# Kernel optimization log

Measured on AMD Instinct MI355X. Metric: run time of the kernel, lower is better.

## Reference

```python
import jax, jax.numpy as jnp
import numpy as np

R = 12          # resolution (H = W = G); L = R**3 = 1728
HEADS = 12


def setup_inputs() -> dict:
    key = jax.random.key(0)
    k1, k2, k3 = jax.random.split(key, 3)
    B, L, C = 4, R ** 3, 768
    qkv = jax.random.normal(k1, (3, B, L, C), dtype=jnp.float32)
    lepe_w = jax.random.normal(k2, (C, 1, 3, 3, 3), dtype=jnp.float32) * 0.05
    lepe_b = jax.random.normal(k3, (C,), dtype=jnp.float32) * 0.01
    return {"qkv": qkv, "lepe_w": lepe_w, "lepe_b": lepe_b}


def reference(qkv, lepe_w, lepe_b):
    # qkv: [3, B, L, C]; idx=0 => window == full volume, so attention is dense over L.
    q, k, v = qkv[0], qkv[1], qkv[2]
    B, L, C = q.shape
    hd = C // HEADS
    scale = hd ** -0.5

    # im2cswin with full-volume window preserves token order: [B, L, C] -> [B, H, L, d]
    qh = q.reshape(B, L, HEADS, hd).transpose(0, 2, 1, 3)
    kh = k.reshape(B, L, HEADS, hd).transpose(0, 2, 1, 3)

    # get_lepe: v -> [B, C, R, R, R], depthwise 3x3x3 conv (groups=C)
    v_img = v.transpose(0, 2, 1).reshape(B, C, R, R, R)
    lepe = jax.lax.conv_general_dilated(
        v_img, lepe_w, window_strides=(1, 1, 1), padding="SAME",
        dimension_numbers=("NCDHW", "OIDHW", "NCDHW"), feature_group_count=C,
    ) + lepe_b[None, :, None, None, None]
    lepe = lepe.reshape(B, HEADS, hd, L).transpose(0, 1, 3, 2)   # [B, H, L, d]
    vh = v_img.reshape(B, HEADS, hd, L).transpose(0, 1, 3, 2)    # [B, H, L, d]

    attn = jax.nn.softmax(jnp.einsum("bhqd,bhkd->bhqk", qh * scale, kh), axis=-1)
    out = jnp.einsum("bhqk,bhkd->bhqd", attn, vh) + lepe          # [B, H, L, d]

    # windows2img with full window is an inverse reshape back to [B, L, C]
    return out.transpose(0, 2, 1, 3).reshape(B, L, C)
```

## Files before the change

kernel.cpp:

```cpp
#include <hip/hip_runtime.h>

#define RR 12
#define LL 1728
#define CC 768
#define HEADS 12
#define HD 64
#define BATCH 4

typedef __attribute__((ext_vector_type(8))) short bf8;
typedef __attribute__((ext_vector_type(4))) float f4;

__device__ inline unsigned short f2bf(float x) {
  unsigned int u = __float_as_uint(x);
  return (unsigned short)((u + 0x7FFFu + ((u >> 16) & 1u)) >> 16);
}
__device__ inline unsigned short f2bfr(float x) {
  return (unsigned short)((__float_as_uint(x) + 0x8000u) >> 16);
}

__device__ inline float fast_exp2(float x) {
#if __has_builtin(__builtin_amdgcn_exp2f)
  return __builtin_amdgcn_exp2f(x);
#else
  return exp2f(x);
#endif
}

__device__ inline void gld16(const unsigned short* g, unsigned short* l) {
  __builtin_amdgcn_global_load_lds((const __attribute__((address_space(1))) unsigned int*)g,
                                   (__attribute__((address_space(3))) unsigned int*)l, 16, 0, 0);
}

#define QSCALE 0.1803368801111244f

__global__ __launch_bounds__(256) void prep_kernel(const float* __restrict__ qkv,
                                                   unsigned short* __restrict__ qb,
                                                   unsigned short* __restrict__ kb,
                                                   unsigned short* __restrict__ vT) {
  __shared__ unsigned short tl[64 * 65];
  const int lt = blockIdx.x;
  const int h = blockIdx.y;
  const int b = blockIdx.z;
  const int t = threadIdx.x;

  {
    const int r0 = t >> 4;
    const int c4 = (t & 15) * 4;
#pragma unroll
    for (int p = 0; p < 4; ++p) {
      const int row = lt * 64 + p * 16 + r0;
      const size_t off = ((size_t)b * LL + row) * CC + h * HD + c4;
      const float4 qv = *(const float4*)(qkv + off);
      ushort4 oq;
      oq.x = f2bf(qv.x * QSCALE); oq.y = f2bf(qv.y * QSCALE);
      oq.z = f2bf(qv.z * QSCALE); oq.w = f2bf(qv.w * QSCALE);
      *(ushort4*)(qb + off) = oq;
      const float4 kv = *(const float4*)(qkv + (size_t)BATCH * LL * CC + off);
      ushort4 ok;
      ok.x = f2bf(kv.x); ok.y = f2bf(kv.y); ok.z = f2bf(kv.z); ok.w = f2bf(kv.w);
      *(ushort4*)(kb + off) = ok;
    }
  }

  const float* vsrc = qkv + ((size_t)(2 * BATCH + b)) * LL * CC;
#pragma unroll
  for (int it = 0; it < 4; ++it) {
    const int idx = it * 256 + t;
    const int lrow = idx >> 4;
    const int c4 = (idx & 15) * 4;
    const float4 vv = *(const float4*)(vsrc + (size_t)(lt * 64 + lrow) * CC + h * HD + c4);
    tl[(c4 + 0) * 65 + lrow] = f2bf(vv.x);
    tl[(c4 + 1) * 65 + lrow] = f2bf(vv.y);
    tl[(c4 + 2) * 65 + lrow] = f2bf(vv.z);
    tl[(c4 + 3) * 65 + lrow] = f2bf(vv.w);
  }
  __syncthreads();
#pragma unroll
  for (int it = 0; it < 4; ++it) {
    const int idx = it * 256 + t;
    const int drow = idx >> 4;
    const int s4 = (idx & 15) * 4;
    const int lb = s4 >> 2;
    ushort4 o;
    o.x = tl[drow * 65 + lb];
    o.y = tl[drow * 65 + 16 + lb];
    o.z = tl[drow * 65 + 32 + lb];
    o.w = tl[drow * 65 + 48 + lb];
    *(ushort4*)(vT + (((size_t)(b * HEADS + h) * HD + drow) * LL) + lt * 64 + s4) = o;
  }
}

__global__ __launch_bounds__(256) void lepe_kernel(const float* __restrict__ qkv,
                                                   const float* __restrict__ w,
                                                   const float* __restrict__ bias,
                                                   float* __restrict__ out) {
  __shared__ float w_lds[256 * 27];

  const int z = blockIdx.x / RR;
  const int y = blockIdx.x % RR;
  const int c0 = blockIdx.y * 256;
  const int c = c0 + threadIdx.x;
  const int b = blockIdx.z;
  const float* vb = qkv + ((size_t)(2 * BATCH + b)) * LL * CC + c;

  {
    const float* wsrc = w + (size_t)c0 * 27;
#pragma unroll
    for (int i = 0; i < 7; ++i) {
      const int idx = i * 256 + threadIdx.x;
      if (idx < 1728)
        *(float4*)&w_lds[idx * 4] = *(const float4*)&wsrc[idx * 4];
    }
  }
  __syncthreads();

  float wreg[27];
#pragma unroll
  for (int j = 0; j < 27; ++j) wreg[j] = w_lds[threadIdx.x * 27 + j];
  const float bv = bias[c];

  int loff[9];
  bool lval[9];
#pragma unroll
  for (int dz = 0; dz < 3; ++dz)
#pragma unroll
    for (int dy = 0; dy < 3; ++dy) {
      const int i = dz * 3 + dy;
      const int zz = z + dz - 1, yy = y + dy - 1;
      lval[i] = (zz >= 0 && zz < RR && yy >= 0 && yy < RR);
      loff[i] = lval[i] ? ((zz * RR + yy) * RR) * CC : 0;
    }

  float prev[9], cur[9], nxt[9];
#pragma unroll
  for (int i = 0; i < 9; ++i) {
    prev[i] = 0.f;
    cur[i] = lval[i] ? vb[loff[i]] : 0.f;
    nxt[i] = lval[i] ? vb[loff[i] + CC] : 0.f;
  }

  const size_t obase = ((size_t)b * LL + (z * RR + y) * RR) * CC + c;
#pragma unroll
  for (int x = 0; x < RR; ++x) {
    float acc = bv;
#pragma unroll
    for (int i = 0; i < 9; ++i)
      acc += wreg[i * 3] * prev[i] + wreg[i * 3 + 1] * cur[i] + wreg[i * 3 + 2] * nxt[i];
    out[obase + (size_t)x * CC] = acc;
#pragma unroll
    for (int i = 0; i < 9; ++i) {
      prev[i] = cur[i];
      cur[i] = nxt[i];
      nxt[i] = (x + 2 < RR && lval[i]) ? vb[loff[i] + (x + 2) * CC] : 0.f;
    }
  }
}

__global__ __launch_bounds__(256) void attn_kernel(const unsigned short* __restrict__ qb,
                                                   const unsigned short* __restrict__ kb,
                                                   const unsigned short* __restrict__ vT,
                                                   float* __restrict__ out) {
  __shared__ unsigned short k_lds[2][64 * 64];
  __shared__ unsigned short v_lds[2][64 * 64];
  __shared__ unsigned short p_lds[4][16 * 72];

  const int qt = blockIdx.x;
  const int h = blockIdx.y;
  const int b = blockIdx.z;
  const int t = threadIdx.x;
  const int lane = t & 63;
  const int wave = t >> 6;
  const int m = lane & 15;
  const int quad = lane >> 4;

  bf8 qf[2];
  {
    const size_t qbase = ((size_t)(b * LL + qt * 64 + wave * 16 + m)) * CC + h * HD;
    qf[0] = *(const bf8*)(qb + qbase + quad * 8);
    qf[1] = *(const bf8*)(qb + qbase + 32 + quad * 8);
  }

  int koff[2], voff[2], ldsb[2];
#pragma unroll
  for (int j = 0; j < 2; ++j) {
    const int cidx = (j * 4 + wave) * 64 + lane;
    const int row = cidx >> 3;
    const int sc = (cidx & 7) ^ (row & 7);
    koff[j] = row * CC + sc * 8;
    voff[j] = row * LL + sc * 8;
    ldsb[j] = (j * 4 + wave) * 512;
  }

  const unsigned short* kgb = kb + (size_t)b * LL * CC + h * HD;
  const unsigned short* vgb = vT + ((size_t)(b * HEADS + h) * HD) * LL;

  gld16(kgb + koff[0], &k_lds[0][ldsb[0]]);
  gld16(kgb + koff[1], &k_lds[0][ldsb[1]]);
  gld16(vgb + voff[0], &v_lds[0][ldsb[0]]);
  gld16(vgb + voff[1], &v_lds[0][ldsb[1]]);

  f4 o_acc[4] = {};
  float psum[4] = {0.f, 0.f, 0.f, 0.f};

#define ATTN_BODY(KT, CUR)                                                              \
  {                                                                                     \
    __syncthreads();            \
    if ((KT) < 26) {                                                                    \
      const size_t ko = (size_t)((KT) + 1) * 64 * CC;                                   \
      const int vo = ((KT) + 1) * 64;                                                   \
      gld16(kgb + ko + koff[0], &k_lds[(CUR) ^ 1][ldsb[0]]);                            \
      gld16(kgb + ko + koff[1], &k_lds[(CUR) ^ 1][ldsb[1]]);                            \
      gld16(vgb + vo + voff[0], &v_lds[(CUR) ^ 1][ldsb[0]]);                            \
      gld16(vgb + vo + voff[1], &v_lds[(CUR) ^ 1][ldsb[1]]);                            \
    }                                                                                   \
    f4 s_acc[4] = {};                                                                   \
    _Pragma("unroll")                                                                   \
    for (int nt = 0; nt < 4; ++nt) {                                                    \
      _Pragma("unroll")                                                                 \
      for (int ks = 0; ks < 2; ++ks) {                                                  \
        const int cc = ((ks * 4 + quad) ^ (m & 7)) * 8;                                 \
        const bf8 kf = *(const bf8*)&k_lds[CUR][(nt * 16 + m) * 64 + cc];               \
        s_acc[nt] = __builtin_amdgcn_mfma_f32_16x16x32_bf16(qf[ks], kf, s_acc[nt], 0, 0, 0); \
      }                                                                                 \
    }                                                                                   \
    _Pragma("unroll")                                                                   \
    for (int r = 0; r < 4; ++r) {                                                       \
      const float p0 = fast_exp2(s_acc[0][r]);                                          \
      const float p1 = fast_exp2(s_acc[1][r]);                                          \
      const float p2 = fast_exp2(s_acc[2][r]);                                          \
      const float p3 = fast_exp2(s_acc[3][r]);                                          \
      psum[r] += (p0 + p1) + (p2 + p3);                                                 \
      ushort4 pk;        \
      pk.x = f2bfr(p0); pk.y = f2bfr(p1); pk.z = f2bfr(p2); pk.w = f2bfr(p3);           \
      *(ushort4*)&p_lds[wave][(quad * 4 + r) * 72 + m * 4] = pk;                        \
    }                                                                                   \
    __asm__ volatile("s_waitcnt lgkmcnt(0)" ::: "memory");      \
    bf8 pf[2];                                                                          \
    _Pragma("unroll")                                                                   \
    for (int ks = 0; ks < 2; ++ks)                                                      \
      pf[ks] = *(const bf8*)&p_lds[wave][m * 72 + ks * 32 + quad * 8];                  \
    _Pragma("unroll")                                                                   \
    for (int nt = 0; nt < 4; ++nt) {                                                    \
      _Pragma("unroll")                                                                 \
      for (int ks = 0; ks < 2; ++ks) {                                                  \
        const int cc = ((ks * 4 + quad) ^ (m & 7)) * 8;                                 \
        const bf8 vf = *(const bf8*)&v_lds[CUR][(nt * 16 + m) * 64 + cc];               \
        o_acc[nt] = __builtin_amdgcn_mfma_f32_16x16x32_bf16(pf[ks], vf, o_acc[nt], 0, 0, 0); \
      }                                                                                 \
    }                                                                                   \
  }

  for (int ktp = 0; ktp < 13; ++ktp) {
    const int kt0 = ktp * 2;
    ATTN_BODY(kt0, 0)
    ATTN_BODY(kt0 + 1, 1)
  }
  ATTN_BODY(26, 0)
#undef ATTN_BODY

#pragma unroll
  for (int r = 0; r < 4; ++r) {
    float s = psum[r];
    s += __shfl_xor(s, 1);
    s += __shfl_xor(s, 2);
    s += __shfl_xor(s, 4);
    s += __shfl_xor(s, 8);
    const float inv = 1.0f / s;
    const int row = qt * 64 + wave * 16 + quad * 4 + r;
    float* op = out + ((size_t)b * LL + row) * CC + h * HD;
#pragma unroll
    for (int nt = 0; nt < 4; ++nt) {
      const int cix = nt * 16 + m;
      op[cix] = op[cix] + o_acc[nt][r] * inv;
    }
  }
}

extern "C" void kernel_launch(void* const* d_in, const int* in_sizes, int n_in,
                              void* d_out, int out_size, void* d_ws, size_t ws_size,
                              hipStream_t stream) {
  (void)in_sizes; (void)n_in; (void)ws_size; (void)out_size;
  const float* qkv = (const float*)d_in[0];
  const float* lepe_w = (const float*)d_in[1];
  const float* lepe_b = (const float*)d_in[2];
  float* out = (float*)d_out;

  const size_t NE = (size_t)BATCH * LL * CC;
  unsigned short* qb = (unsigned short*)d_ws;
  unsigned short* kb = qb + NE;
  unsigned short* vT = kb + NE;

  prep_kernel<<<dim3(27, HEADS, BATCH), 256, 0, stream>>>(qkv, qb, kb, vT);
  lepe_kernel<<<dim3(RR * RR, CC / 256, BATCH), 256, 0, stream>>>(qkv, lepe_w, lepe_b, out);
  attn_kernel<<<dim3(27, HEADS, BATCH), 256, 0, stream>>>(qb, kb, vT, out);
}
```

Measured before the change: 195.6 us.

## Fuse depthwise LePE convolution into the attention kernel's key-tile loop

New measurement: 275.5 us. 1.41x slower.

```diff
diff --git a/kernel.cpp b/kernel.cpp
--- a/kernel.cpp
+++ b/kernel.cpp
@@ -90,79 +90,17 @@
   }
 }
 
-__global__ __launch_bounds__(256) void lepe_kernel(const float* __restrict__ qkv,
-                                                   const float* __restrict__ w,
-                                                   const float* __restrict__ bias,
-                                                   float* __restrict__ out) {
-  __shared__ float w_lds[256 * 27];
-
-  const int z = blockIdx.x / RR;
-  const int y = blockIdx.x % RR;
-  const int c0 = blockIdx.y * 256;
-  const int c = c0 + threadIdx.x;
-  const int b = blockIdx.z;
-  const float* vb = qkv + ((size_t)(2 * BATCH + b)) * LL * CC + c;
-
-  {
-    const float* wsrc = w + (size_t)c0 * 27;
-#pragma unroll
-    for (int i = 0; i < 7; ++i) {
-      const int idx = i * 256 + threadIdx.x;
-      if (idx < 1728)
-        *(float4*)&w_lds[idx * 4] = *(const float4*)&wsrc[idx * 4];
-    }
-  }
-  __syncthreads();
-
-  float wreg[27];
-#pragma unroll
-  for (int j = 0; j < 27; ++j) wreg[j] = w_lds[threadIdx.x * 27 + j];
-  const float bv = bias[c];
-
-  int loff[9];
-  bool lval[9];
-#pragma unroll
-  for (int dz = 0; dz < 3; ++dz)
-#pragma unroll
-    for (int dy = 0; dy < 3; ++dy) {
-      const int i = dz * 3 + dy;
-      const int zz = z + dz - 1, yy = y + dy - 1;
-      lval[i] = (zz >= 0 && zz < RR && yy >= 0 && yy < RR);
-      loff[i] = lval[i] ? ((zz * RR + yy) * RR) * CC : 0;
-    }
-
-  float prev[9], cur[9], nxt[9];
-#pragma unroll
-  for (int i = 0; i < 9; ++i) {
-    prev[i] = 0.f;
-    cur[i] = lval[i] ? vb[loff[i]] : 0.f;
-    nxt[i] = lval[i] ? vb[loff[i] + CC] : 0.f;
-  }
-
-  const size_t obase = ((size_t)b * LL + (z * RR + y) * RR) * CC + c;
-#pragma unroll
-  for (int x = 0; x < RR; ++x) {
-    float acc = bv;
-#pragma unroll
-    for (int i = 0; i < 9; ++i)
-      acc += wreg[i * 3] * prev[i] + wreg[i * 3 + 1] * cur[i] + wreg[i * 3 + 2] * nxt[i];
-    out[obase + (size_t)x * CC] = acc;
-#pragma unroll
-    for (int i = 0; i < 9; ++i) {
-      prev[i] = cur[i];
-      cur[i] = nxt[i];
-      nxt[i] = (x + 2 < RR && lval[i]) ? vb[loff[i] + (x + 2) * CC] : 0.f;
-    }
-  }
-}
-
 __global__ __launch_bounds__(256) void attn_kernel(const unsigned short* __restrict__ qb,
                                                    const unsigned short* __restrict__ kb,
                                                    const unsigned short* __restrict__ vT,
+                                                   const float* __restrict__ qkv,
+                                                   const float* __restrict__ w,
+                                                   const float* __restrict__ bias,
                                                    float* __restrict__ out) {
   __shared__ unsigned short k_lds[2][64 * 64];
   __shared__ unsigned short v_lds[2][64 * 64];
   __shared__ unsigned short p_lds[4][16 * 72];
+  __shared__ float w_lds[64 * 27];
 
   const int qt = blockIdx.x;
   const int h = blockIdx.y;
@@ -180,6 +118,15 @@
     qf[1] = *(const bf8*)(qb + qbase + 32 + quad * 8);
   }
 
+  {
+    const float* wsrc = w + (size_t)h * HD * 27;
+#pragma unroll
+    for (int i = 0; i < 2; ++i) {
+      const int idx = i * 256 + t;
+      if (idx < 432) *(float4*)&w_lds[idx * 4] = *(const float4*)&wsrc[idx * 4];
+    }
+  }
+
   int koff[2], voff[2], ldsb[2];
 #pragma unroll
   for (int j = 0; j < 2; ++j) {
@@ -194,12 +141,23 @@
   const unsigned short* kgb = kb + (size_t)b * LL * CC + h * HD;
   const unsigned short* vgb = vT + ((size_t)(b * HEADS + h) * HD) * LL;
 
+  int zr[4], yr[4], xr[4];
+#pragma unroll
+  for (int r = 0; r < 4; ++r) {
+    const int l = qt * 64 + wave * 16 + quad * 4 + r;
+    zr[r] = l / (RR * RR);
+    yr[r] = (l / RR) % RR;
+    xr[r] = l % RR;
+  }
+  const float* vconv = qkv + ((size_t)(2 * BATCH + b)) * LL * CC + h * HD + m;
+
   gld16(kgb + koff[0], &k_lds[0][ldsb[0]]);
   gld16(kgb + koff[1], &k_lds[0][ldsb[1]]);
   gld16(vgb + voff[0], &v_lds[0][ldsb[0]]);
   gld16(vgb + voff[1], &v_lds[0][ldsb[1]]);
 
   f4 o_acc[4] = {};
+  f4 lepe[4] = {};
   float psum[4] = {0.f, 0.f, 0.f, 0.f};
 
 #define ATTN_BODY(KT, CUR)                                                              \
@@ -223,6 +181,21 @@
         s_acc[nt] = __builtin_amdgcn_mfma_f32_16x16x32_bf16(qf[ks], kf, s_acc[nt], 0, 0, 0); \
       }                                                                                 \
     }                                                                                   \
+    {                 \
+      const int dz = (KT) / 9 - 1, dy = ((KT) % 9) / 3 - 1, dx = (KT) % 3 - 1;          \
+      float wv[4];                                                                      \
+      _Pragma("unroll")                                                                 \
+      for (int nt = 0; nt < 4; ++nt) wv[nt] = w_lds[(nt * 16 + m) * 27 + (KT)];         \
+      _Pragma("unroll")                                                                 \
+      for (int r = 0; r < 4; ++r) {                                                     \
+        const int zz = zr[r] + dz, yy = yr[r] + dy, xx = xr[r] + dx;                    \
+        if (((unsigned)zz < RR) & ((unsigned)yy < RR) & ((unsigned)xx < RR)) {          \
+          const float* vrow = vconv + (size_t)((zz * RR + yy) * RR + xx) * CC;          \
+          _Pragma("unroll")                                                             \
+          for (int nt = 0; nt < 4; ++nt) lepe[nt][r] += wv[nt] * vrow[nt * 16];         \
+        }                                                                               \
+      }                                                                                 \
+    }                                                                                   \
     _Pragma("unroll")                                                                   \
     for (int r = 0; r < 4; ++r) {                                                       \
       const float p0 = fast_exp2(s_acc[0][r]);                                          \
@@ -258,6 +231,9 @@
   ATTN_BODY(26, 0)
 #undef ATTN_BODY
 
+  float bv[4];
+#pragma unroll
+  for (int nt = 0; nt < 4; ++nt) bv[nt] = bias[h * HD + nt * 16 + m];
 #pragma unroll
   for (int r = 0; r < 4; ++r) {
     float s = psum[r];
@@ -269,10 +245,8 @@
     const int row = qt * 64 + wave * 16 + quad * 4 + r;
     float* op = out + ((size_t)b * LL + row) * CC + h * HD;
 #pragma unroll
-    for (int nt = 0; nt < 4; ++nt) {
-      const int cix = nt * 16 + m;
-      op[cix] = op[cix] + o_acc[nt][r] * inv;
-    }
+    for (int nt = 0; nt < 4; ++nt)
+      op[nt * 16 + m] = o_acc[nt][r] * inv + lepe[nt][r] + bv[nt];
   }
 }
 
@@ -291,6 +265,5 @@
   unsigned short* vT = kb + NE;
 
   prep_kernel<<<dim3(27, HEADS, BATCH), 256, 0, stream>>>(qkv, qb, kb, vT);
-  lepe_kernel<<<dim3(RR * RR, CC / 256, BATCH), 256, 0, stream>>>(qkv, lepe_w, lepe_b, out);
-  attn_kernel<<<dim3(27, HEADS, BATCH), 256, 0, stream>>>(qb, kb, vT, out);
-}
+  attn_kernel<<<dim3(27, HEADS, BATCH), 256, 0, stream>>>(qb, kb, vT, qkv, lepe_w, lepe_b, out);
+}
```
